# Optimization experiments

Measured on AMD Instinct MI355X. Metric: run time of the kernel, lower is better.

The kernel has to match this reference:

```python
import jax, jax.numpy as jnp
import numpy as np

EMBED_DIM = 1024
NUM_HEADS = 16
D_K = EMBED_DIM // NUM_HEADS


def setup_inputs() -> dict:
    key = jax.random.key(0)
    ks = jax.random.split(key, 9)
    B, T, C = 4, 2048, EMBED_DIM
    s = 1.0 / np.sqrt(C)
    inp = {
        "x": jax.random.normal(ks[0], (B, T, C), dtype=jnp.float32),
        "Wq": jax.random.uniform(ks[1], (C, C), jnp.float32, -s, s),
        "bq": jax.random.uniform(ks[2], (C,), jnp.float32, -s, s),
        "Wk": jax.random.uniform(ks[3], (C, C), jnp.float32, -s, s),
        "bk": jax.random.uniform(ks[4], (C,), jnp.float32, -s, s),
        "Wv": jax.random.uniform(ks[5], (C, C), jnp.float32, -s, s),
        "bv": jax.random.uniform(ks[6], (C,), jnp.float32, -s, s),
        "Wo": jax.random.uniform(ks[7], (C, C), jnp.float32, -s, s),
        "bo": jax.random.uniform(ks[8], (C,), jnp.float32, -s, s),
    }
    return inp


def reference(x, Wq, bq, Wk, bk, Wv, bv, Wo, bo):
    B, T, C = x.shape
    H, Dk = NUM_HEADS, D_K
    # torch Linear: y = x @ W.T + b
    def proj(W, b):
        y = jnp.einsum('btc,dc->btd', x, W) + b
        return y.reshape(B, T, H, Dk).transpose(0, 2, 1, 3)  # [B,H,T,Dk]
    q = proj(Wq, bq)
    k = proj(Wk, bk)
    v = proj(Wv, bv)
    scores = jnp.einsum('bhtd,bhsd->bhts', q, k) / jnp.sqrt(jnp.float32(Dk))
    attn = jax.nn.softmax(scores, axis=-1)
    ctx = jnp.einsum('bhts,bhsd->bhtd', attn, v)
    ctx = ctx.transpose(0, 2, 1, 3).reshape(B, T, C)
    return jnp.einsum('btc,dc->btd', ctx, Wo) + bo
```

## Files before the change

### kernel.cpp

```cpp
#include <hip/hip_runtime.h>
#include <hip/hip_bf16.h>
#include <cstdint>

using u16 = unsigned short;
typedef __attribute__((ext_vector_type(8))) short short8;
typedef __attribute__((ext_vector_type(8))) _Float16 f16x8;
typedef __attribute__((ext_vector_type(4))) float floatx4;

#define MFMA16(a, b, c) __builtin_amdgcn_mfma_f32_16x16x32_bf16((a), (b), (c), 0, 0, 0)
#define MFMAH(a, b, c)  __builtin_amdgcn_mfma_f32_16x16x32_f16((a), (b), (c), 0, 0, 0)

#define GLL(gp, lp) __builtin_amdgcn_global_load_lds( \
    (const __attribute__((address_space(1))) unsigned int*)(gp), \
    (__attribute__((address_space(3))) unsigned int*)(lp), 16, 0, 0)

__device__ __forceinline__ u16 f2bf(float f) {
    union { float f; unsigned u; } v; v.f = f;
    return (u16)((v.u + 0x7FFFu + ((v.u >> 16) & 1u)) >> 16);
}
__device__ __forceinline__ u16 f2h(float f) {
    _Float16 h = (_Float16)f;
    return __builtin_bit_cast(u16, h);
}
__device__ __forceinline__ unsigned cvt_pk_bf16(float lo, float hi) {
    unsigned r;
    asm("v_cvt_pk_bf16_f32 %0, %1, %2" : "=v"(r) : "v"(lo), "v"(hi));
    return r;
}
__device__ __forceinline__ float fast_exp2(float x) {
#if __has_builtin(__builtin_amdgcn_exp2f)
    return __builtin_amdgcn_exp2f(x);
#else
    float r; asm("v_exp_f32 %0, %1" : "=v"(r) : "v"(x)); return r;
#endif
}
__device__ __forceinline__ float fast_rcp(float x) {
#if __has_builtin(__builtin_amdgcn_rcpf)
    return __builtin_amdgcn_rcpf(x);
#else
    float r; asm("v_rcp_f32 %0, %1" : "=v"(r) : "v"(x)); return r;
#endif
}

__global__ void cast_x_f16(const float* __restrict__ src, u16* __restrict__ dst, int n4) {
    int idx = blockIdx.x * blockDim.x + threadIdx.x;
    int stride = gridDim.x * blockDim.x;
    for (int i = idx; i < n4; i += stride) {
        float4 v = reinterpret_cast<const float4*>(src)[i];
        reinterpret_cast<ushort4*>(dst)[i] =
            make_ushort4(f2h(v.x), f2h(v.y), f2h(v.z), f2h(v.w));
    }
}

__global__ void cast_w_f16(const float* q, const float* k, const float* v, const float* o,
                           u16* q16, u16* k16, u16* v16, u16* o16, int n4) {
    const float* src; u16* dst;
    switch (blockIdx.y) {
        case 0:  src = q; dst = q16; break;
        case 1:  src = k; dst = k16; break;
        case 2:  src = v; dst = v16; break;
        default: src = o; dst = o16; break;
    }
    int idx = blockIdx.x * blockDim.x + threadIdx.x;
    int stride = gridDim.x * blockDim.x;
    for (int i = idx; i < n4; i += stride) {
        float4 w = reinterpret_cast<const float4*>(src)[i];
        reinterpret_cast<ushort4*>(dst)[i] =
            make_ushort4(f2h(w.x), f2h(w.y), f2h(w.z), f2h(w.w));
    }
}

__device__ __forceinline__ void gemm_core(
    const u16* __restrict__ A16, const u16* __restrict__ B16,
    const float* __restrict__ bias, u16* __restrict__ out16,
    float* __restrict__ outf, int mode, float scale, char* ldsb) {
    int flat = blockIdx.x + (blockIdx.y << 6);
    int swz = (flat & 7) * 64 + (flat >> 3);
    const int m0 = ((swz >> 6) * 8 + ((swz >> 3) & 7)) << 7;
    const int n0 = (swz & 7) << 7;

    const int t = threadIdx.x, lane = t & 63, w = t >> 6;
    const int c = lane & 15, g = lane >> 4;
    const int wm = w & 1, wn = w >> 1;

    floatx4 zero = {0.f, 0.f, 0.f, 0.f};
    floatx4 acc[4][4];
#pragma unroll
    for (int mf = 0; mf < 4; ++mf)
#pragma unroll
        for (int nf = 0; nf < 4; ++nf) acc[mf][nf] = zero;

    const u16* gsrc[2] = {A16 + (size_t)m0 * 1024, B16 + (size_t)n0 * 1024};

    int dst_db[4];
    size_t src_el[4];
#pragma unroll
    for (int j = 0; j < 4; ++j) {
        int db = t * 16 + j * 4096;
        int local = db & 8191;
        int row = local >> 6;
        int colsw = (local & 63) ^ (((local >> 7) & 3) << 4);
        dst_db[j] = db;
        src_el[j] = (size_t)row * 1024 + (colsw >> 1);
    }

    int offA[4], offB[4];
#pragma unroll
    for (int f = 0; f < 4; ++f) {
        int rA = wm * 64 + f * 16 + c;
        offA[f] = rA * 64 + ((g * 16) ^ (((rA >> 1) & 3) << 4));
        int rB = wn * 64 + f * 16 + c;
        offB[f] = 8192 + rB * 64 + ((g * 16) ^ (((rB >> 1) & 3) << 4));
    }

#define GSTAGE(BUF, K0) do { \
    _Pragma("unroll") \
    for (int j = 0; j < 4; ++j) \
        GLL(gsrc[j >> 1] + src_el[j] + (K0), ldsb + (BUF) * 16384 + dst_db[j]); \
    } while (0)

    GSTAGE(0, 0);
    for (int k0 = 0; k0 < 1024; k0 += 32) {
        const int cur = (k0 >> 5) & 1;
        __syncthreads();
        if (k0 + 32 < 1024) GSTAGE(cur ^ 1, k0 + 32);
        const char* lb = ldsb + cur * 16384;

        f16x8 a[4], b[4];
#pragma unroll
        for (int f = 0; f < 4; ++f) {
            a[f] = *reinterpret_cast<const f16x8*>(lb + offA[f]);
            b[f] = *reinterpret_cast<const f16x8*>(lb + offB[f]);
        }
#pragma unroll
        for (int mf = 0; mf < 4; ++mf)
#pragma unroll
            for (int nf = 0; nf < 4; ++nf)
                acc[mf][nf] = MFMAH(a[mf], b[nf], acc[mf][nf]);
    }
#undef GSTAGE

#pragma unroll
    for (int nf = 0; nf < 4; ++nf) {
        int col = n0 + wn * 64 + nf * 16 + c;
        float bv = bias[col];
#pragma unroll
        for (int mf = 0; mf < 4; ++mf) {
            int rb = m0 + wm * 64 + mf * 16 + 4 * g;
            if (mode == 2) {
#pragma unroll
                for (int i = 0; i < 4; ++i)
                    outf[(size_t)(rb + i) * 1024 + col] = (acc[mf][nf][i] + bv) * scale;
            } else {
                int b = rb >> 11, tt = rb & 2047, h = col >> 6, dk = col & 63;
                if (mode == 0) {
#pragma unroll
                    for (int i = 0; i < 4; ++i)
                        out16[((size_t)(b * 16 + h) * 2048 + tt + i) * 64 + dk] =
                            f2bf((acc[mf][nf][i] + bv) * scale);
                } else {
                    ushort4 pk;
                    pk.x = f2bf((acc[mf][nf][0] + bv) * scale);
                    pk.y = f2bf((acc[mf][nf][1] + bv) * scale);
                    pk.z = f2bf((acc[mf][nf][2] + bv) * scale);
                    pk.w = f2bf((acc[mf][nf][3] + bv) * scale);
                    int k64 = tt & 63, q = k64 >> 4, sub = (k64 >> 2) & 3;
                    int pos = ((q >> 1) << 5) + (sub << 3) + ((q & 1) << 2);
                    *reinterpret_cast<ushort4*>(
                        out16 + ((size_t)(b * 16 + h) * 64 + dk) * 2048 +
                        (tt & ~63) + pos) = pk;
                }
            }
        }
    }
}

__global__ __launch_bounds__(256) void gemm_qkv(
    const u16* __restrict__ x16,
    const u16* __restrict__ Wq, const u16* __restrict__ Wk, const u16* __restrict__ Wv,
    const float* __restrict__ bq, const float* __restrict__ bk, const float* __restrict__ bv,
    u16* __restrict__ Qb, u16* __restrict__ Kb, u16* __restrict__ Vtb, float qscale) {
    __shared__ __align__(16) char lds[2][16384];
    if (blockIdx.z == 0)      gemm_core(x16, Wq, bq, Qb,  nullptr, 0, qscale, (char*)lds);
    else if (blockIdx.z == 1) gemm_core(x16, Wk, bk, Kb,  nullptr, 0, 1.0f, (char*)lds);
    else                      gemm_core(x16, Wv, bv, Vtb, nullptr, 1, 1.0f, (char*)lds);
}

__global__ __launch_bounds__(256) void gemm_o(
    const u16* __restrict__ cx, const u16* __restrict__ Wo,
    const float* __restrict__ bo, float* __restrict__ out) {
    __shared__ __align__(16) char lds[2][16384];
    gemm_core(cx, Wo, bo, nullptr, out, 2, 1.0f, (char*)lds);
}

__global__ __launch_bounds__(512) void attn_flash(
    const u16* __restrict__ Q, const u16* __restrict__ K, const u16* __restrict__ Vt,
    u16* __restrict__ ctx) {
    __shared__ __align__(16) char kv_lds[2][16384];

    int flat = blockIdx.x + (blockIdx.y << 4);
    int swz = (flat & 7) * 128 + (flat >> 3);
    const int q0 = (swz & 15) << 7;
    const int bh = swz >> 4;

    const int lane = threadIdx.x & 63, w = threadIdx.x >> 6;
    const int c = lane & 15, g = lane >> 4;

    const u16* qrow = Q + ((size_t)bh * 2048 + q0 + w * 16 + c) * 64;
    short8 qf0 = *reinterpret_cast<const short8*>(qrow + g * 8);
    short8 qf1 = *reinterpret_cast<const short8*>(qrow + 32 + g * 8);

    const bool isK = (w < 4);
    const char* sptr = isK ? (const char*)(K + (size_t)bh * 2048 * 64)
                           : (const char*)(Vt + (size_t)bh * 64 * 2048);
    const int sadv = isK ? 8192 : 128;
    size_t src_off[2];
    int dst_off[2];
#pragma unroll
    for (int j = 0; j < 2; ++j) {
        int base = (w & 3) * 2048 + j * 1024 + lane * 16;
        int row = base >> 7, col = (base & 127) ^ ((row & 7) << 4);
        if (isK) { dst_off[j] = base;        src_off[j] = (size_t)row * 128  + col; }
        else     { dst_off[j] = 8192 + base; src_off[j] = (size_t)row * 4096 + col; }
    }

    const int sw = (c & 7) << 4;
    const int abase0 = c * 128 + ((g * 16) ^ sw);
    const int abase1 = c * 128 + ((64 + g * 16) ^ sw);

    short8 ones;
#pragma unroll
    for (int e = 0; e < 8; ++e) ones[e] = (short)0x3F80;

    floatx4 zero = {0.f, 0.f, 0.f, 0.f};
    floatx4 acc[4] = {zero, zero, zero, zero};
    floatx4 acc5 = zero;

    union pa_t { unsigned u[4]; short8 s; };
    pa_t paA0, paA1, paB0, paB1;
    short8 vrA[8], vrB[8];

#define STAGE_TO(BUF) do { \
    GLL(sptr + src_off[0], (char*)kv_lds + (BUF) * 16384 + dst_off[0]); \
    GLL(sptr + src_off[1], (char*)kv_lds + (BUF) * 16384 + dst_off[1]); \
    sptr += sadv; } while (0)

#define PHASE(BUF, PAc0, PAc1, VRc, PAp0, PAp1, VRp, DO_PV, DO_STAGE, SBUF) do { \
    __syncthreads(); \
    if (DO_STAGE) STAGE_TO(SBUF); \
    const char* kbL = (const char*)kv_lds + (BUF) * 16384; \
    floatx4 st[4]; \
    __builtin_amdgcn_s_setprio(1); \
    _Pragma("unroll") \
    for (int kf = 0; kf < 4; ++kf) { \
        short8 k0 = *reinterpret_cast<const short8*>(kbL + kf * 2048 + abase0); \
        short8 k1 = *reinterpret_cast<const short8*>(kbL + kf * 2048 + abase1); \
        st[kf] = MFMA16(k1, qf1, MFMA16(k0, qf0, zero)); \
    } \
    if (DO_PV) { \
        acc5 = MFMA16(PAp0.s, ones, acc5); \
        acc5 = MFMA16(PAp1.s, ones, acc5); \
        _Pragma("unroll") \
        for (int nt = 0; nt < 4; ++nt) \
            acc[nt] = MFMA16(PAp1.s, VRp[nt + 4], MFMA16(PAp0.s, VRp[nt], acc[nt])); \
    } \
    __builtin_amdgcn_s_setprio(0); \
    _Pragma("unroll") \
    for (int nt = 0; nt < 4; ++nt) { \
        VRc[nt]     = *reinterpret_cast<const short8*>(kbL + 8192 + nt * 2048 + abase0); \
        VRc[nt + 4] = *reinterpret_cast<const short8*>(kbL + 8192 + nt * 2048 + abase1); \
    } \
    float p[4][4]; \
    _Pragma("unroll") \
    for (int kf = 0; kf < 4; ++kf) \
        _Pragma("unroll") \
        for (int i = 0; i < 4; ++i) p[kf][i] = fast_exp2(st[kf][i]); \
    PAc0.u[0] = cvt_pk_bf16(p[0][0], p[0][1]); \
    PAc0.u[1] = cvt_pk_bf16(p[0][2], p[0][3]); \
    PAc0.u[2] = cvt_pk_bf16(p[1][0], p[1][1]); \
    PAc0.u[3] = cvt_pk_bf16(p[1][2], p[1][3]); \
    PAc1.u[0] = cvt_pk_bf16(p[2][0], p[2][1]); \
    PAc1.u[1] = cvt_pk_bf16(p[2][2], p[2][3]); \
    PAc1.u[2] = cvt_pk_bf16(p[3][0], p[3][1]); \
    PAc1.u[3] = cvt_pk_bf16(p[3][2], p[3][3]); \
    } while (0)

    STAGE_TO(0);
    PHASE(0, paA0, paA1, vrA, paB0, paB1, vrB, 0, 1, 1);
    for (int it = 0; it < 15; ++it) {
        PHASE(1, paB0, paB1, vrB, paA0, paA1, vrA, 1, 1, 0);
        PHASE(0, paA0, paA1, vrA, paB0, paB1, vrB, 1, 1, 1);
    }
    PHASE(1, paB0, paB1, vrB, paA0, paA1, vrA, 1, 0, 0);
    acc5 = MFMA16(paB0.s, ones, acc5);
    acc5 = MFMA16(paB1.s, ones, acc5);
#pragma unroll
    for (int nt = 0; nt < 4; ++nt)
        acc[nt] = MFMA16(paB1.s, vrB[nt + 4], MFMA16(paB0.s, vrB[nt], acc[nt]));
#undef STAGE_TO
#undef PHASE

    const int b = bh >> 4, h = bh & 15;
    float rl[4];
#pragma unroll
    for (int i = 0; i < 4; ++i) rl[i] = fast_rcp(acc5[i]);
#pragma unroll
    for (int nt = 0; nt < 4; ++nt) {
#pragma unroll
        for (int i = 0; i < 4; ++i) {
            int tt = q0 + w * 16 + 4 * g + i;
            size_t idx = ((size_t)b * 2048 + tt) * 1024 + h * 64 + nt * 16 + c;
            ctx[idx] = f2h(acc[nt][i] * rl[i]);
        }
    }
}

extern "C" void kernel_launch(void* const* d_in, const int* in_sizes, int n_in,
                              void* d_out, int out_size, void* d_ws, size_t ws_size,
                              hipStream_t stream) {
    if (n_in < 9) return;
    const float* x  = (const float*)d_in[0];
    const float* Wq = (const float*)d_in[1];
    const float* bq = (const float*)d_in[2];
    const float* Wk = (const float*)d_in[3];
    const float* bk = (const float*)d_in[4];
    const float* Wv = (const float*)d_in[5];
    const float* bv = (const float*)d_in[6];
    const float* Wo = (const float*)d_in[7];
    const float* bo = (const float*)d_in[8];
    float* out = (float*)d_out;

    const size_t NX = 8192ull * 1024ull;
    const size_t NW = 1024ull * 1024ull;
    u16* p = (u16*)d_ws;
    u16* x16  = p; p += NX;
    u16* Wq16 = p; p += NW;
    u16* Wk16 = p; p += NW;
    u16* Wv16 = p; p += NW;
    u16* Wo16 = p; p += NW;
    u16* Qb   = p; p += NX;
    u16* Kb   = p; p += NX;
    u16* Vtb  = p; p += NX;
    u16* cx   = p; p += NX;
    if ((size_t)((char*)p - (char*)d_ws) > ws_size) return;

    dim3 blk(256);
    cast_x_f16<<<dim3(2048), blk, 0, stream>>>(x, x16, (int)(NX / 4));
    cast_w_f16<<<dim3(256, 4), blk, 0, stream>>>(
        Wq, Wk, Wv, Wo, Wq16, Wk16, Wv16, Wo16, (int)(NW / 4));

    const float qscale = 0.125f * 1.44269504088896f;
    gemm_qkv<<<dim3(64, 8, 3), blk, 0, stream>>>(
        x16, Wq16, Wk16, Wv16, bq, bk, bv, Qb, Kb, Vtb, qscale);

    attn_flash<<<dim3(16, 64), dim3(512), 0, stream>>>(Qb, Kb, Vtb, cx);

    gemm_o<<<dim3(64, 8), blk, 0, stream>>>(cx, Wo16, bo, out);
}
```

Measured before the change: 170.8 us.

## Deepen LDS pipelines to four buffers with prefetch distance two and explicit vmcnt waits

Result: slower. 180.9 us (+5.9%).

```diff
diff --git a/kernel.cpp b/kernel.cpp
--- a/kernel.cpp
+++ b/kernel.cpp
@@ -13,6 +13,11 @@
 #define GLL(gp, lp) __builtin_amdgcn_global_load_lds( \
     (const __attribute__((address_space(1))) unsigned int*)(gp), \
     (__attribute__((address_space(3))) unsigned int*)(lp), 16, 0, 0)
+
+#define WAITBAR(N) do { \
+    asm volatile("s_waitcnt vmcnt(" #N ")" ::: "memory"); \
+    __builtin_amdgcn_s_barrier(); \
+    __builtin_amdgcn_sched_barrier(0); } while (0)
 
 __device__ __forceinline__ u16 f2bf(float f) {
     union { float f; unsigned u; } v; v.f = f;
@@ -120,11 +125,17 @@
     } while (0)
 
     GSTAGE(0, 0);
-    for (int k0 = 0; k0 < 1024; k0 += 32) {
-        const int cur = (k0 >> 5) & 1;
-        __syncthreads();
-        if (k0 + 32 < 1024) GSTAGE(cur ^ 1, k0 + 32);
-        const char* lb = ldsb + cur * 16384;
+    GSTAGE(1, 32);
+    for (int k = 0; k < 32; ++k) {
+        if (k == 31) {
+            asm volatile("s_waitcnt vmcnt(0)" ::: "memory");
+        } else {
+            asm volatile("s_waitcnt vmcnt(4)" ::: "memory");
+        }
+        __builtin_amdgcn_s_barrier();
+        __builtin_amdgcn_sched_barrier(0);
+        if (k + 2 < 32) GSTAGE((k + 2) & 3, (k + 2) * 32);
+        const char* lb = ldsb + (k & 3) * 16384;
 
         f16x8 a[4], b[4];
 #pragma unroll
@@ -180,7 +191,7 @@
     const u16* __restrict__ Wq, const u16* __restrict__ Wk, const u16* __restrict__ Wv,
     const float* __restrict__ bq, const float* __restrict__ bk, const float* __restrict__ bv,
     u16* __restrict__ Qb, u16* __restrict__ Kb, u16* __restrict__ Vtb, float qscale) {
-    __shared__ __align__(16) char lds[2][16384];
+    __shared__ __align__(16) char lds[4][16384];
     if (blockIdx.z == 0)      gemm_core(x16, Wq, bq, Qb,  nullptr, 0, qscale, (char*)lds);
     else if (blockIdx.z == 1) gemm_core(x16, Wk, bk, Kb,  nullptr, 0, 1.0f, (char*)lds);
     else                      gemm_core(x16, Wv, bv, Vtb, nullptr, 1, 1.0f, (char*)lds);
@@ -189,14 +200,14 @@
 __global__ __launch_bounds__(256) void gemm_o(
     const u16* __restrict__ cx, const u16* __restrict__ Wo,
     const float* __restrict__ bo, float* __restrict__ out) {
-    __shared__ __align__(16) char lds[2][16384];
+    __shared__ __align__(16) char lds[4][16384];
     gemm_core(cx, Wo, bo, nullptr, out, 2, 1.0f, (char*)lds);
 }
 
 __global__ __launch_bounds__(512) void attn_flash(
     const u16* __restrict__ Q, const u16* __restrict__ K, const u16* __restrict__ Vt,
     u16* __restrict__ ctx) {
-    __shared__ __align__(16) char kv_lds[2][16384];
+    __shared__ __align__(16) char kv_lds[4][16384];
 
     int flat = blockIdx.x + (blockIdx.y << 4);
     int swz = (flat & 7) * 128 + (flat >> 3);
@@ -245,8 +256,8 @@
     GLL(sptr + src_off[1], (char*)kv_lds + (BUF) * 16384 + dst_off[1]); \
     sptr += sadv; } while (0)
 
-#define PHASE(BUF, PAc0, PAc1, VRc, PAp0, PAp1, VRp, DO_PV, DO_STAGE, SBUF) do { \
-    __syncthreads(); \
+#define PHASE(N, BUF, SBUF, DO_STAGE, PAc0, PAc1, VRc, PAp0, PAp1, VRp, DO_PV) do { \
+    WAITBAR(N); \
     if (DO_STAGE) STAGE_TO(SBUF); \
     const char* kbL = (const char*)kv_lds + (BUF) * 16384; \
     floatx4 st[4]; \
@@ -286,12 +297,21 @@
     } while (0)
 
     STAGE_TO(0);
-    PHASE(0, paA0, paA1, vrA, paB0, paB1, vrB, 0, 1, 1);
-    for (int it = 0; it < 15; ++it) {
-        PHASE(1, paB0, paB1, vrB, paA0, paA1, vrA, 1, 1, 0);
-        PHASE(0, paA0, paA1, vrA, paB0, paB1, vrB, 1, 1, 1);
-    }
-    PHASE(1, paB0, paB1, vrB, paA0, paA1, vrA, 1, 0, 0);
+    STAGE_TO(1);
+    PHASE(2, 0, 2, 1, paA0, paA1, vrA, paB0, paB1, vrB, 0);
+    PHASE(2, 1, 3, 1, paB0, paB1, vrB, paA0, paA1, vrA, 1);
+    PHASE(2, 2, 0, 1, paA0, paA1, vrA, paB0, paB1, vrB, 1);
+    PHASE(2, 3, 1, 1, paB0, paB1, vrB, paA0, paA1, vrA, 1);
+    for (int it = 0; it < 6; ++it) {
+        PHASE(2, 0, 2, 1, paA0, paA1, vrA, paB0, paB1, vrB, 1);
+        PHASE(2, 1, 3, 1, paB0, paB1, vrB, paA0, paA1, vrA, 1);
+        PHASE(2, 2, 0, 1, paA0, paA1, vrA, paB0, paB1, vrB, 1);
+        PHASE(2, 3, 1, 1, paB0, paB1, vrB, paA0, paA1, vrA, 1);
+    }
+    PHASE(2, 0, 2, 1, paA0, paA1, vrA, paB0, paB1, vrB, 1);
+    PHASE(2, 1, 3, 1, paB0, paB1, vrB, paA0, paA1, vrA, 1);
+    PHASE(2, 2, 0, 0, paA0, paA1, vrA, paB0, paB1, vrB, 1);
+    PHASE(0, 3, 1, 0, paB0, paB1, vrB, paA0, paA1, vrA, 1);
     acc5 = MFMA16(paB0.s, ones, acc5);
     acc5 = MFMA16(paB1.s, ones, acc5);
 #pragma unroll
```
